# Optimization experiments

Hardware: AMD Instinct MI355X
Metric: run time of the kernel (lower is better)

## Reference

```python
import jax, jax.numpy as jnp
import numpy as np

N = 50000      # node_num
F = 128        # input_dim
D = 128        # output_dim
K = 4          # len(support): Lanczos depth and number of weight matrices
E = 800000     # n_edges = N * avg_degree(16)
EPS = 1e-12    # tf.nn.l2_normalize epsilon


def setup_inputs() -> dict:
    key = jax.random.key(0)
    k1, k2, k3, k4, k5 = jax.random.split(key, 5)
    x = jax.random.normal(k1, (N, F), dtype=jnp.float32)
    edge_vals = jax.random.uniform(k2, (E,), dtype=jnp.float32)
    weights = jax.random.normal(k3, (K, F, D), dtype=jnp.float32) * 0.05
    edge_row = jax.random.randint(k4, (E,), 0, N, dtype=jnp.int32)
    edge_col = jax.random.randint(k5, (E,), 0, N, dtype=jnp.int32)
    return {"x": x, "edge_vals": edge_vals, "weights": weights,
            "edge_row": edge_row, "edge_col": edge_col}


def reference(x, edge_vals, weights, edge_row, edge_col):
    # x: [N, F] node features; sparse operator A with A[row, col] = val.
    # Original loops Lanczos per feature column; here all F columns run in parallel.
    n = x.shape[0]
    k = weights.shape[0]

    def spmv(v):  # A @ v for v: [N, F]
        return jax.ops.segment_sum(edge_vals[:, None] * v[edge_col], edge_row,
                                   num_segments=n)

    # v0 = l2_normalize of each feature column (tf.nn.l2_normalize semantics)
    v0 = x * jax.lax.rsqrt(jnp.maximum(jnp.sum(x * x, axis=0, keepdims=True), EPS))

    def step(carry, _):
        v_prev, v_prev2, beta_prev = carry
        w = spmv(v_prev)                                        # [N, F]
        alpha = jnp.sum(w * v_prev, axis=0, keepdims=True)      # [1, F]
        new_v = w - alpha * v_prev - beta_prev * v_prev2        # beta_prev=0 on step 1
        beta = jnp.sqrt(jnp.sum(new_v * new_v, axis=0, keepdims=True))  # [1, F]
        v = new_v / beta
        return (v, v_prev, beta), v

    init = (v0, jnp.zeros_like(v0), jnp.zeros((1, x.shape[1]), x.dtype))
    _, vs = jax.lax.scan(step, init, None, length=k - 1)        # [K-1, N, F]
    Vs = jnp.concatenate([v0[None], vs], axis=0)                # [K, N, F]

    # sum_j Vm_matrix[j] @ W_j, then relu (bias=False)
    out = jnp.einsum('knf,kfd->nd', Vs, weights)                # [N, D]
    return jax.nn.relu(out)
```

## Files before the change

### kernel.cpp

```cpp
#include <hip/hip_runtime.h>

#define F128 128
#define EPSV 1e-12f

typedef short bf16x8 __attribute__((ext_vector_type(8)));
typedef float f32x4 __attribute__((ext_vector_type(4)));
typedef unsigned short u16x4 __attribute__((ext_vector_type(4)));

static __device__ __forceinline__ unsigned short f2bf(float f) {
  unsigned u = __float_as_uint(f);
  u += 0x7FFF + ((u >> 16) & 1);
  return (unsigned short)(u >> 16);
}
static __device__ __forceinline__ float bf2f(unsigned short b) {
  return __uint_as_float(((unsigned)b) << 16);
}

__global__ void hist_kernel(const int* __restrict__ row, int* __restrict__ counts, int E) {
  int i = blockIdx.x * blockDim.x + threadIdx.x;
  int stride = gridDim.x * blockDim.x;
  for (; i < E; i += stride) atomicAdd(&counts[row[i]], 1);
}

__global__ __launch_bounds__(1024) void scan_local_kernel(const int* __restrict__ counts,
                                                          int* __restrict__ tmp,
                                                          int* __restrict__ partials, int n) {
  __shared__ int buf[1024];
  int t = threadIdx.x;
  int i = blockIdx.x * 1024 + t;
  int v = (i < n) ? counts[i] : 0;
  buf[t] = v;
  __syncthreads();
  for (int off = 1; off < 1024; off <<= 1) {
    int add = (t >= off) ? buf[t - off] : 0;
    __syncthreads();
    buf[t] += add;
    __syncthreads();
  }
  if (i < n) tmp[i] = buf[t];
  if (t == 1023) partials[blockIdx.x] = buf[1023];
}

__global__ __launch_bounds__(256) void scan_part_kernel(const int* __restrict__ partials,
                                                        int* __restrict__ part_excl, int nblk) {
  __shared__ int buf[256];
  int t = threadIdx.x;
  int v = (t < nblk) ? partials[t] : 0;
  buf[t] = v;
  __syncthreads();
  for (int off = 1; off < 256; off <<= 1) {
    int add = (t >= off) ? buf[t - off] : 0;
    __syncthreads();
    buf[t] += add;
    __syncthreads();
  }
  if (t < nblk) part_excl[t] = buf[t] - v;
}

__global__ __launch_bounds__(1024) void scan_fin_kernel(const int* __restrict__ tmp,
                                                        const int* __restrict__ part_excl,
                                                        const int* __restrict__ counts,
                                                        int* __restrict__ row_ptr,
                                                        int* __restrict__ fill, int n) {
  int t = threadIdx.x;
  int i = blockIdx.x * 1024 + t;
  if (i < n) {
    int incl = tmp[i] + part_excl[blockIdx.x];
    row_ptr[i + 1] = incl;
    fill[i] = incl - counts[i];
  }
  if (i == 0) row_ptr[0] = 0;
}

__global__ void scatter_kernel(const int* __restrict__ row, const int* __restrict__ col,
                               const float* __restrict__ val, int* __restrict__ fill,
                               int2* __restrict__ edges, int E, int N) {
  int part = blockIdx.x & 7;
  int g = blockIdx.x >> 3;
  int stride = (gridDim.x >> 3) * blockDim.x;
  int lo = (int)(((long long)N * part) >> 3);
  int hi = (int)(((long long)N * (part + 1)) >> 3);
  for (int i = g * blockDim.x + threadIdx.x; i < E; i += stride) {
    int r = row[i];
    if (r >= lo && r < hi) {
      int pos = atomicAdd(&fill[r], 1);
      edges[pos] = make_int2(col[i], __float_as_int(val[i]));
    }
  }
}

__global__ __launch_bounds__(256) void reduce_cols_kernel(const float* __restrict__ part,
                                                          float* __restrict__ out, int P) {
  __shared__ float red[256];
  int f = blockIdx.x;
  int t = threadIdx.x;
  float s = 0.f;
  for (int p = t; p < P; p += 256) s += part[(size_t)p * F128 + f];
  red[t] = s;
  __syncthreads();
  for (int off = 128; off > 0; off >>= 1) {
    if (t < off) red[t] += red[t + off];
    __syncthreads();
  }
  if (t == 0) out[f] = red[0];
}

__global__ __launch_bounds__(256) void spmv_dot_kernel(const int* __restrict__ row_ptr,
                                                       const int2* __restrict__ edges,
                                                       const unsigned short* __restrict__ ubf,
                                                       const float* __restrict__ raw, float eps,
                                                       unsigned short* __restrict__ wbf,
                                                       float* __restrict__ dot_part, int N) {
  __shared__ float part[4][F128];
  int wv = threadIdx.x >> 6, lane = threadIdx.x & 63;
  int row0 = (blockIdx.x * 4 + wv) * 4;
  float rin0 = rsqrtf(fmaxf(raw[lane * 2 + 0], eps));
  float rin1 = rsqrtf(fmaxf(raw[lane * 2 + 1], eps));
  float dx = 0.f, dy = 0.f;
#pragma unroll 1
  for (int r = 0; r < 4; ++r) {
    int wid = row0 + r;
    if (wid >= N) break;
    int beg = row_ptr[wid], end = row_ptr[wid + 1];
    float ax0 = 0.f, ay0 = 0.f, ax1 = 0.f, ay1 = 0.f;
    float ax2 = 0.f, ay2 = 0.f, ax3 = 0.f, ay3 = 0.f;
    int e = beg;
    for (; e + 4 <= end; e += 4) {
      int eu = __builtin_amdgcn_readfirstlane(e);
      int2 e0 = edges[eu + 0];
      int2 e1 = edges[eu + 1];
      int2 e2 = edges[eu + 2];
      int2 e3 = edges[eu + 3];
      unsigned b0 = *(const unsigned*)&ubf[(size_t)e0.x * F128 + lane * 2];
      unsigned b1 = *(const unsigned*)&ubf[(size_t)e1.x * F128 + lane * 2];
      unsigned b2 = *(const unsigned*)&ubf[(size_t)e2.x * F128 + lane * 2];
      unsigned b3 = *(const unsigned*)&ubf[(size_t)e3.x * F128 + lane * 2];
      float s0 = __int_as_float(e0.y), s1 = __int_as_float(e1.y);
      float s2 = __int_as_float(e2.y), s3 = __int_as_float(e3.y);
      ax0 += s0 * __uint_as_float(b0 << 16);
      ay0 += s0 * __uint_as_float(b0 & 0xffff0000u);
      ax1 += s1 * __uint_as_float(b1 << 16);
      ay1 += s1 * __uint_as_float(b1 & 0xffff0000u);
      ax2 += s2 * __uint_as_float(b2 << 16);
      ay2 += s2 * __uint_as_float(b2 & 0xffff0000u);
      ax3 += s3 * __uint_as_float(b3 << 16);
      ay3 += s3 * __uint_as_float(b3 & 0xffff0000u);
    }
    for (; e < end; ++e) {
      int eu = __builtin_amdgcn_readfirstlane(e);
      int2 ee = edges[eu];
      unsigned bb = *(const unsigned*)&ubf[(size_t)ee.x * F128 + lane * 2];
      float ss = __int_as_float(ee.y);
      ax0 += ss * __uint_as_float(bb << 16);
      ay0 += ss * __uint_as_float(bb & 0xffff0000u);
    }
    float ox = ((ax0 + ax1) + (ax2 + ax3)) * rin0;
    float oy = ((ay0 + ay1) + (ay2 + ay3)) * rin1;
    unsigned packed = ((unsigned)f2bf(oy) << 16) | (unsigned)f2bf(ox);
    *(unsigned*)&wbf[(size_t)wid * F128 + lane * 2] = packed;
    unsigned ub = *(const unsigned*)&ubf[(size_t)wid * F128 + lane * 2];
    dx += ox * __uint_as_float(ub << 16) * rin0;
    dy += oy * __uint_as_float(ub & 0xffff0000u) * rin1;
  }
  part[wv][lane * 2 + 0] = dx;
  part[wv][lane * 2 + 1] = dy;
  __syncthreads();
  if (threadIdx.x < F128) {
    float s = part[0][threadIdx.x] + part[1][threadIdx.x] +
              part[2][threadIdx.x] + part[3][threadIdx.x];
    dot_part[(size_t)blockIdx.x * F128 + threadIdx.x] = s;
  }
}

__global__ __launch_bounds__(256) void colsq_kernel(const float* __restrict__ a,
                                                    unsigned short* __restrict__ abf,
                                                    float* __restrict__ part, int nrows) {
  int t = threadIdx.x;
  int f0 = (t & 31) * 4;
  int rslot = blockIdx.x * 8 + (t >> 5);
  int rstride = gridDim.x * 8;
  float4 acc = make_float4(0.f, 0.f, 0.f, 0.f);
  for (int r = rslot; r < nrows; r += rstride) {
    size_t idx = (size_t)r * F128 + f0;
    float4 av = *(const float4*)&a[idx];
    ushort4 bv;
    bv.x = f2bf(av.x); bv.y = f2bf(av.y); bv.z = f2bf(av.z); bv.w = f2bf(av.w);
    *(ushort4*)&abf[idx] = bv;
    acc.x += av.x * av.x; acc.y += av.y * av.y;
    acc.z += av.z * av.z; acc.w += av.w * av.w;
  }
  __shared__ float4 red[256];
  red[t] = acc;
  __syncthreads();
  if (t < 32) {
    float4 s = red[t];
#pragma unroll
    for (int j = 1; j < 8; ++j) {
      float4 o = red[t + 32 * j];
      s.x += o.x; s.y += o.y; s.z += o.z; s.w += o.w;
    }
    *(float4*)&part[(size_t)blockIdx.x * F128 + t * 4] = s;
  }
}

template <int HAS_PREV>
__global__ __launch_bounds__(256) void newv_kernel(const unsigned short* __restrict__ wbf,
                                                   unsigned short* __restrict__ outbf,
                                                   const unsigned short* __restrict__ upbf,
                                                   const unsigned short* __restrict__ up2bf,
                                                   const float* __restrict__ alpha,
                                                   const float* __restrict__ prev_raw, float prev_eps,
                                                   const float* __restrict__ prev2_raw, float prev2_eps,
                                                   float* __restrict__ bsq_part, int nrows) {
  int t = threadIdx.x;
  int f0 = (t & 31) * 4;
  int rslot = blockIdx.x * 8 + (t >> 5);
  int rstride = gridDim.x * 8;
  float4 a = *(const float4*)&alpha[f0];
  float4 pr = *(const float4*)&prev_raw[f0];
  float4 cp;
  cp.x = rsqrtf(fmaxf(pr.x, prev_eps)); cp.y = rsqrtf(fmaxf(pr.y, prev_eps));
  cp.z = rsqrtf(fmaxf(pr.z, prev_eps)); cp.w = rsqrtf(fmaxf(pr.w, prev_eps));
  float4 ac;
  ac.x = a.x * cp.x; ac.y = a.y * cp.y; ac.z = a.z * cp.z; ac.w = a.w * cp.w;
  float4 g = make_float4(0.f, 0.f, 0.f, 0.f);
  if (HAS_PREV) {
    float4 p2 = *(const float4*)&prev2_raw[f0];
    g.x = sqrtf(pr.x) * rsqrtf(fmaxf(p2.x, prev2_eps));
    g.y = sqrtf(pr.y) * rsqrtf(fmaxf(p2.y, prev2_eps));
    g.z = sqrtf(pr.z) * rsqrtf(fmaxf(p2.z, prev2_eps));
    g.w = sqrtf(pr.w) * rsqrtf(fmaxf(p2.w, prev2_eps));
  }
  float4 acc = make_float4(0.f, 0.f, 0.f, 0.f);
  for (int r = rslot; r < nrows; r += rstride) {
    size_t idx = (size_t)r * F128 + f0;
    ushort4 wb = *(const ushort4*)&wbf[idx];
    float4 wv;
    wv.x = bf2f(wb.x); wv.y = bf2f(wb.y); wv.z = bf2f(wb.z); wv.w = bf2f(wb.w);
    ushort4 pb = *(const ushort4*)&upbf[idx];
    wv.x -= ac.x * bf2f(pb.x);
    wv.y -= ac.y * bf2f(pb.y);
    wv.z -= ac.z * bf2f(pb.z);
    wv.w -= ac.w * bf2f(pb.w);
    if (HAS_PREV) {
      ushort4 qb = *(const ushort4*)&up2bf[idx];
      wv.x -= g.x * bf2f(qb.x);
      wv.y -= g.y * bf2f(qb.y);
      wv.z -= g.z * bf2f(qb.z);
      wv.w -= g.w * bf2f(qb.w);
    }
    u16x4 ob;
    ob.x = f2bf(wv.x); ob.y = f2bf(wv.y); ob.z = f2bf(wv.z); ob.w = f2bf(wv.w);
    *(u16x4*)&outbf[idx] = ob;
    acc.x += wv.x * wv.x; acc.y += wv.y * wv.y;
    acc.z += wv.z * wv.z; acc.w += wv.w * wv.w;
  }
  __shared__ float4 red[256];
  red[t] = acc;
  __syncthreads();
  if (t < 32) {
    float4 s = red[t];
#pragma unroll
    for (int j = 1; j < 8; ++j) {
      float4 o = red[t + 32 * j];
      s.x += o.x; s.y += o.y; s.z += o.z; s.w += o.w;
    }
    *(float4*)&bsq_part[(size_t)blockIdx.x * F128 + t * 4] = s;
  }
}

__global__ void wprep_kernel(const float* __restrict__ weights,
                             const float* __restrict__ norms,
                             const float* __restrict__ betasq,
                             unsigned short* __restrict__ wfrag, int total) {
  int t = blockIdx.x * blockDim.x + threadIdx.x;
  if (t >= total) return;
  int k = t >> 14;
  int f = (t >> 7) & 127;
  int d = t & 127;
  float c = (k == 0) ? rsqrtf(fmaxf(norms[f], EPSV)) : rsqrtf(betasq[(k - 1) * F128 + f]);
  float val = weights[t] * c;
  int Kidx = k * F128 + f;
  int kstep = Kidx >> 5, kin = Kidx & 31;
  int lane = ((kin >> 3) << 4) | (d & 15);
  int ct = d >> 4, j = kin & 7;
  wfrag[(((kstep * 8 + ct) * 64 + lane) << 3) | j] = f2bf(val);
}

__global__ __launch_bounds__(256) void mfma_gemm_kernel(float* __restrict__ out,
                                                        const unsigned short* __restrict__ xbf,
                                                        const unsigned short* __restrict__ ubfs,
                                                        size_t nf,
                                                        const unsigned short* __restrict__ wfrag,
                                                        int N, int K) {
  int wv = threadIdx.x >> 6, lane = threadIdx.x & 63;
  int n0 = blockIdx.x * 64 + wv * 16;
  if (n0 >= N) return;
  int rrow = n0 + (lane & 15);
  if (rrow >= N) rrow = N - 1;
  int khalf = lane >> 4;
  f32x4 acc[8];
#pragma unroll
  for (int i = 0; i < 8; ++i) acc[i] = (f32x4){0.f, 0.f, 0.f, 0.f};
  for (int k = 0; k < K; ++k) {
    const unsigned short* Uk = (k == 0) ? xbf : (ubfs + (size_t)(k - 1) * nf);
    const unsigned short* arow = Uk + (size_t)rrow * F128 + khalf * 8;
#pragma unroll
    for (int kk = 0; kk < 4; ++kk) {
      bf16x8 af = *(const bf16x8*)(arow + kk * 32);
      int kstep = k * 4 + kk;
      const unsigned short* bbase = wfrag + (((kstep * 8) * 64 + lane) << 3);
#pragma unroll
      for (int ct = 0; ct < 8; ++ct) {
        bf16x8 bfr = *(const bf16x8*)(bbase + (ct << 9));
        acc[ct] = __builtin_amdgcn_mfma_f32_16x16x32_bf16(af, bfr, acc[ct], 0, 0, 0);
      }
    }
  }
#pragma unroll
  for (int ct = 0; ct < 8; ++ct) {
#pragma unroll
    for (int j = 0; j < 4; ++j) {
      int r = n0 + khalf * 4 + j;
      if (r < N) out[(size_t)r * F128 + ct * 16 + (lane & 15)] = fmaxf(acc[ct][j], 0.f);
    }
  }
}

extern "C" void kernel_launch(void* const* d_in, const int* in_sizes, int n_in,
                              void* d_out, int out_size, void* d_ws, size_t ws_size,
                              hipStream_t stream) {
  const float* x = (const float*)d_in[0];
  const float* edge_vals = (const float*)d_in[1];
  const float* weights = (const float*)d_in[2];
  const int* edge_row = (const int*)d_in[3];
  const int* edge_col = (const int*)d_in[4];

  const int N = in_sizes[0] / F128;
  const int E = in_sizes[1];
  const int K = in_sizes[2] / (F128 * F128);
  float* out = (float*)d_out;

  size_t nf = (size_t)N * F128;
  int spmv_blocks = (N + 15) / 16;
  const int RB = 2048;

  unsigned short* wbf = (unsigned short*)d_ws;
  unsigned short* xbf = wbf + nf;
  unsigned short* ubfs = xbf + nf;
  unsigned short* wfrag = ubfs + (size_t)(K - 1) * nf;
  int wtotal = K * F128 * F128;
  int* row_ptr = (int*)(wfrag + wtotal);
  int* fill = row_ptr + (N + 2);
  int* counts = fill + N;
  int* tmp = counts + N;
  int* partials = tmp + N;
  int* part_excl = partials + 256;
  int2* edges = (int2*)(part_excl + 256);
  float* dot_part = (float*)(edges + E);
  float* col_part = dot_part + (size_t)spmv_blocks * F128;
  float* norms = col_part + (size_t)RB * F128;
  float* alpha = norms + F128;
  float* betasq = alpha + 8 * F128;

  hipMemsetAsync(counts, 0, (size_t)N * sizeof(int), stream);

  int nblk = (N + 1023) / 1024;
  hist_kernel<<<1024, 256, 0, stream>>>(edge_row, counts, E);
  scan_local_kernel<<<nblk, 1024, 0, stream>>>(counts, tmp, partials, N);
  scan_part_kernel<<<1, 256, 0, stream>>>(partials, part_excl, nblk);
  scan_fin_kernel<<<nblk, 1024, 0, stream>>>(tmp, part_excl, counts, row_ptr, fill, N);
  scatter_kernel<<<2048, 256, 0, stream>>>(edge_row, edge_col, edge_vals, fill, edges, E, N);

  colsq_kernel<<<RB, 256, 0, stream>>>(x, xbf, col_part, N);
  reduce_cols_kernel<<<F128, 256, 0, stream>>>(col_part, norms, RB);

  const unsigned short* ubf_prev = xbf;
  const unsigned short* ubf_prev2 = nullptr;
  const float* praw = norms;
  float peps = EPSV;
  const float* p2raw = nullptr;
  float p2eps = 0.f;
  for (int s = 1; s < K; ++s) {
    unsigned short* ubf_out = ubfs + (size_t)(s - 1) * nf;
    float* alph = alpha + (size_t)(s - 1) * F128;
    float* bsq = betasq + (size_t)(s - 1) * F128;

    spmv_dot_kernel<<<spmv_blocks, 256, 0, stream>>>(row_ptr, edges, ubf_prev, praw, peps,
                                                     wbf, dot_part, N);
    reduce_cols_kernel<<<F128, 256, 0, stream>>>(dot_part, alph, spmv_blocks);
    if (s == 1)
      newv_kernel<0><<<RB, 256, 0, stream>>>(wbf, ubf_out, ubf_prev, nullptr, alph, praw, peps,
                                             nullptr, 0.f, col_part, N);
    else
      newv_kernel<1><<<RB, 256, 0, stream>>>(wbf, ubf_out, ubf_prev, ubf_prev2, alph, praw, peps,
                                             p2raw, p2eps, col_part, N);
    reduce_cols_kernel<<<F128, 256, 0, stream>>>(col_part, bsq, RB);

    ubf_prev2 = ubf_prev; p2raw = praw; p2eps = peps;
    ubf_prev = ubf_out;   praw = bsq;   peps = 0.f;
  }

  wprep_kernel<<<(wtotal + 255) / 256, 256, 0, stream>>>(weights, norms, betasq, wfrag, wtotal);
  mfma_gemm_kernel<<<(N + 63) / 64, 256, 0, stream>>>(out, xbf, ubfs, nf, wfrag, N, K);
}
```

Baseline: 313.3 us.

## Split SpMV feature columns into quarters so blocks gather narrower rows

```diff
diff --git a/kernel.cpp b/kernel.cpp
--- a/kernel.cpp
+++ b/kernel.cpp
@@ -105,70 +105,112 @@
   if (t == 0) out[f] = red[0];
 }
 
+__global__ __launch_bounds__(256) void reduce_quarter_kernel(const float* __restrict__ part,
+                                                             float* __restrict__ out, int npairs) {
+  __shared__ float red[256];
+  int f = blockIdx.x;
+  int q = f >> 5, fi = f & 31;
+  int t = threadIdx.x;
+  int nb = npairs * 2;
+  float s = 0.f;
+  for (int j = t; j < nb; j += 256) {
+    int g = j >> 1, sub = j & 1;
+    int b = g * 8 + 2 * q + sub;
+    s += part[(size_t)b * 32 + fi];
+  }
+  red[t] = s;
+  __syncthreads();
+  for (int off = 128; off > 0; off >>= 1) {
+    if (t < off) red[t] += red[t + off];
+    __syncthreads();
+  }
+  if (t == 0) out[f] = red[0];
+}
+
 __global__ __launch_bounds__(256) void spmv_dot_kernel(const int* __restrict__ row_ptr,
                                                        const int2* __restrict__ edges,
                                                        const unsigned short* __restrict__ ubf,
                                                        const float* __restrict__ raw, float eps,
                                                        unsigned short* __restrict__ wbf,
-                                                       float* __restrict__ dot_part, int N) {
-  __shared__ float part[4][F128];
+                                                       float* __restrict__ dot_part,
+                                                       int N, int npairs) {
+  __shared__ float part[4][32];
+  int b = blockIdx.x;
+  int x = b & 7, g = b >> 3;
+  int q = x >> 1, sub = x & 1;
+  int j0 = g * 2 + sub;
+  int jstride = npairs * 2;
+  int ntiles = (N + 15) / 16;
   int wv = threadIdx.x >> 6, lane = threadIdx.x & 63;
-  int row0 = (blockIdx.x * 4 + wv) * 4;
-  float rin0 = rsqrtf(fmaxf(raw[lane * 2 + 0], eps));
-  float rin1 = rsqrtf(fmaxf(raw[lane * 2 + 1], eps));
+  int slot = lane >> 4, li = lane & 15;
+  int foff = q * 32 + li * 2;
+  float rin0 = rsqrtf(fmaxf(raw[foff + 0], eps));
+  float rin1 = rsqrtf(fmaxf(raw[foff + 1], eps));
   float dx = 0.f, dy = 0.f;
+  for (int tile = j0; tile < ntiles; tile += jstride) {
+    int row0 = tile * 16 + wv * 4;
 #pragma unroll 1
-  for (int r = 0; r < 4; ++r) {
-    int wid = row0 + r;
-    if (wid >= N) break;
-    int beg = row_ptr[wid], end = row_ptr[wid + 1];
-    float ax0 = 0.f, ay0 = 0.f, ax1 = 0.f, ay1 = 0.f;
-    float ax2 = 0.f, ay2 = 0.f, ax3 = 0.f, ay3 = 0.f;
-    int e = beg;
-    for (; e + 4 <= end; e += 4) {
-      int eu = __builtin_amdgcn_readfirstlane(e);
-      int2 e0 = edges[eu + 0];
-      int2 e1 = edges[eu + 1];
-      int2 e2 = edges[eu + 2];
-      int2 e3 = edges[eu + 3];
-      unsigned b0 = *(const unsigned*)&ubf[(size_t)e0.x * F128 + lane * 2];
-      unsigned b1 = *(const unsigned*)&ubf[(size_t)e1.x * F128 + lane * 2];
-      unsigned b2 = *(const unsigned*)&ubf[(size_t)e2.x * F128 + lane * 2];
-      unsigned b3 = *(const unsigned*)&ubf[(size_t)e3.x * F128 + lane * 2];
-      float s0 = __int_as_float(e0.y), s1 = __int_as_float(e1.y);
-      float s2 = __int_as_float(e2.y), s3 = __int_as_float(e3.y);
-      ax0 += s0 * __uint_as_float(b0 << 16);
-      ay0 += s0 * __uint_as_float(b0 & 0xffff0000u);
-      ax1 += s1 * __uint_as_float(b1 << 16);
-      ay1 += s1 * __uint_as_float(b1 & 0xffff0000u);
-      ax2 += s2 * __uint_as_float(b2 << 16);
-      ay2 += s2 * __uint_as_float(b2 & 0xffff0000u);
-      ax3 += s3 * __uint_as_float(b3 << 16);
-      ay3 += s3 * __uint_as_float(b3 & 0xffff0000u);
-    }
-    for (; e < end; ++e) {
-      int eu = __builtin_amdgcn_readfirstlane(e);
-      int2 ee = edges[eu];
-      unsigned bb = *(const unsigned*)&ubf[(size_t)ee.x * F128 + lane * 2];
-      float ss = __int_as_float(ee.y);
-      ax0 += ss * __uint_as_float(bb << 16);
-      ay0 += ss * __uint_as_float(bb & 0xffff0000u);
-    }
-    float ox = ((ax0 + ax1) + (ax2 + ax3)) * rin0;
-    float oy = ((ay0 + ay1) + (ay2 + ay3)) * rin1;
-    unsigned packed = ((unsigned)f2bf(oy) << 16) | (unsigned)f2bf(ox);
-    *(unsigned*)&wbf[(size_t)wid * F128 + lane * 2] = packed;
-    unsigned ub = *(const unsigned*)&ubf[(size_t)wid * F128 + lane * 2];
-    dx += ox * __uint_as_float(ub << 16) * rin0;
-    dy += oy * __uint_as_float(ub & 0xffff0000u) * rin1;
-  }
-  part[wv][lane * 2 + 0] = dx;
-  part[wv][lane * 2 + 1] = dy;
-  __syncthreads();
-  if (threadIdx.x < F128) {
+    for (int r = 0; r < 4; ++r) {
+      int wid = row0 + r;
+      if (wid >= N) break;
+      int beg = row_ptr[wid], end = row_ptr[wid + 1];
+      float a0x = 0.f, a0y = 0.f, a1x = 0.f, a1y = 0.f;
+      float a2x = 0.f, a2y = 0.f, a3x = 0.f, a3y = 0.f;
+      int e = beg;
+      for (; e + 16 <= end; e += 16) {
+        int2 e0 = edges[e + 0 + slot];
+        int2 e1 = edges[e + 4 + slot];
+        int2 e2 = edges[e + 8 + slot];
+        int2 e3 = edges[e + 12 + slot];
+        unsigned g0 = *(const unsigned*)&ubf[(size_t)e0.x * F128 + foff];
+        unsigned g1 = *(const unsigned*)&ubf[(size_t)e1.x * F128 + foff];
+        unsigned g2 = *(const unsigned*)&ubf[(size_t)e2.x * F128 + foff];
+        unsigned g3 = *(const unsigned*)&ubf[(size_t)e3.x * F128 + foff];
+        float s0 = __int_as_float(e0.y), s1 = __int_as_float(e1.y);
+        float s2 = __int_as_float(e2.y), s3 = __int_as_float(e3.y);
+        a0x += s0 * bf2f((unsigned short)(g0 & 0xffffu));
+        a0y += s0 * bf2f((unsigned short)(g0 >> 16));
+        a1x += s1 * bf2f((unsigned short)(g1 & 0xffffu));
+        a1y += s1 * bf2f((unsigned short)(g1 >> 16));
+        a2x += s2 * bf2f((unsigned short)(g2 & 0xffffu));
+        a2y += s2 * bf2f((unsigned short)(g2 >> 16));
+        a3x += s3 * bf2f((unsigned short)(g3 & 0xffffu));
+        a3y += s3 * bf2f((unsigned short)(g3 >> 16));
+      }
+      for (; e < end; e += 4) {
+        bool ok = (e + slot) < end;
+        int2 ee = ok ? edges[e + slot] : make_int2(0, 0);
+        unsigned gg = *(const unsigned*)&ubf[(size_t)ee.x * F128 + foff];
+        float ss = __int_as_float(ee.y);
+        a0x += ss * bf2f((unsigned short)(gg & 0xffffu));
+        a0y += ss * bf2f((unsigned short)(gg >> 16));
+      }
+      float accx = (a0x + a1x) + (a2x + a3x);
+      float accy = (a0y + a1y) + (a2y + a3y);
+      accx += __shfl_xor(accx, 16);
+      accy += __shfl_xor(accy, 16);
+      accx += __shfl_xor(accx, 32);
+      accy += __shfl_xor(accy, 32);
+      if (slot == 0) {
+        float ox = accx * rin0;
+        float oy = accy * rin1;
+        unsigned pk = ((unsigned)f2bf(oy) << 16) | (unsigned)f2bf(ox);
+        *(unsigned*)&wbf[(size_t)wid * F128 + foff] = pk;
+        unsigned ub = *(const unsigned*)&ubf[(size_t)wid * F128 + foff];
+        dx += ox * bf2f((unsigned short)(ub & 0xffffu)) * rin0;
+        dy += oy * bf2f((unsigned short)(ub >> 16)) * rin1;
+      }
+    }
+  }
+  if (slot == 0) {
+    part[wv][li * 2 + 0] = dx;
+    part[wv][li * 2 + 1] = dy;
+  }
+  __syncthreads();
+  if (threadIdx.x < 32) {
     float s = part[0][threadIdx.x] + part[1][threadIdx.x] +
               part[2][threadIdx.x] + part[3][threadIdx.x];
-    dot_part[(size_t)blockIdx.x * F128 + threadIdx.x] = s;
+    dot_part[(size_t)b * 32 + threadIdx.x] = s;
   }
 }
 
@@ -342,7 +384,8 @@
   float* out = (float*)d_out;
 
   size_t nf = (size_t)N * F128;
-  int spmv_blocks = (N + 15) / 16;
+  const int NPAIRS = 512;
+  const int SPMV_GRID = NPAIRS * 8;
   const int RB = 2048;
 
   unsigned short* wbf = (unsigned short*)d_ws;
@@ -358,7 +401,7 @@
   int* part_excl = partials + 256;
   int2* edges = (int2*)(part_excl + 256);
   float* dot_part = (float*)(edges + E);
-  float* col_part = dot_part + (size_t)spmv_blocks * F128;
+  float* col_part = dot_part + (size_t)SPMV_GRID * 32;
   float* norms = col_part + (size_t)RB * F128;
   float* alpha = norms + F128;
   float* betasq = alpha + 8 * F128;
@@ -386,9 +429,9 @@
     float* alph = alpha + (size_t)(s - 1) * F128;
     float* bsq = betasq + (size_t)(s - 1) * F128;
 
-    spmv_dot_kernel<<<spmv_blocks, 256, 0, stream>>>(row_ptr, edges, ubf_prev, praw, peps,
-                                                     wbf, dot_part, N);
-    reduce_cols_kernel<<<F128, 256, 0, stream>>>(dot_part, alph, spmv_blocks);
+    spmv_dot_kernel<<<SPMV_GRID, 256, 0, stream>>>(row_ptr, edges, ubf_prev, praw, peps,
+                                                   wbf, dot_part, N, NPAIRS);
+    reduce_quarter_kernel<<<F128, 256, 0, stream>>>(dot_part, alph, NPAIRS);
     if (s == 1)
       newv_kernel<0><<<RB, 256, 0, stream>>>(wbf, ubf_out, ubf_prev, nullptr, alph, praw, peps,
                                              nullptr, 0.f, col_part, N);
```

Result: slower. 446.6 us (+42.5%).
